# Performance work log

Hardware: AMD Instinct MI355X
Metric: run time of the kernel (lower is better)

Reference implementation:

```python
import jax, jax.numpy as jnp
import numpy as np

BATCH = 4096
NUM_FEATURES = 2048
DEPTH = 4
KERNEL = 2
THRESHOLD = 0.0


def setup_inputs() -> dict:
    key = jax.random.key(0)
    keys = jax.random.split(key, 2 + 2 * DEPTH + 2)
    inp = {}
    inp['x'] = jax.random.normal(keys[0], (BATCH, NUM_FEATURES), dtype=jnp.float32)
    # Conv2d(1,1,kernel_size=2) weight (k,k) and scalar bias, PyTorch-style init scale
    fan_in = KERNEL * KERNEL
    bound = 1.0 / np.sqrt(fan_in)
    inp['conv_w'] = jax.random.uniform(keys[1], (KERNEL, KERNEL), jnp.float32, -bound, bound)
    inp['conv_b'] = jax.random.uniform(keys[2], (), jnp.float32, -bound, bound)
    # MLP hidden layers
    lb = 1.0 / np.sqrt(NUM_FEATURES)
    for i in range(DEPTH):
        inp[f'W{i}'] = jax.random.uniform(keys[3 + 2 * i], (NUM_FEATURES, NUM_FEATURES), jnp.float32, -lb, lb)
        inp[f'b{i}'] = jax.random.uniform(keys[4 + 2 * i], (NUM_FEATURES,), jnp.float32, -lb, lb)
    inp['Wh'] = jax.random.uniform(keys[3 + 2 * DEPTH], (2, NUM_FEATURES), jnp.float32, -lb, lb)
    inp['bh'] = jax.random.uniform(keys[4 + 2 * DEPTH], (2,), jnp.float32, -lb, lb)
    return inp


def reference(x, conv_w, conv_b, W0, b0, W1, b1, W2, b2, W3, b3, Wh, bh):
    # Per-feature ConvFilter on a constant k x k patch of value x_i collapses to
    # sigmoid(x_i * sum(conv_w) + conv_b - threshold)  -- one fused elementwise op.
    h = jax.nn.sigmoid(x * jnp.sum(conv_w) + conv_b - THRESHOLD)  # (B, F)
    for W, b in ((W0, b0), (W1, b1), (W2, b2), (W3, b3)):
        h = jax.nn.relu(h @ W.T + b)
    return h @ Wh.T + bh  # (B, 2)
```

## Files before the change

kernel.cpp:

```cpp
#include <hip/hip_runtime.h>
#include <math.h>

#define BATCH 4096
#define NF    2048

typedef signed char    i8;
typedef unsigned int   u32;
typedef __attribute__((ext_vector_type(4))) int   intx4;
typedef __attribute__((ext_vector_type(4))) float floatx4;

#define LBW 0.022097086912079612f
#define QMAX 32512.0f
#define AMAX_H 3.0f

__global__ __launch_bounds__(256) void prep_kernel(
    const float* __restrict__ x, const float* __restrict__ cw,
    const float* __restrict__ cb,
    const float* __restrict__ w0, const float* __restrict__ w1,
    const float* __restrict__ w2, const float* __restrict__ w3,
    i8* __restrict__ h1o, i8* __restrict__ h2o,
    i8* __restrict__ q1,  i8* __restrict__ q2)
{
    const int bid = blockIdx.x;
    if (bid < 8192) {
        const float s = cw[0] + cw[1] + cw[2] + cw[3];
        const float c = cb[0];
        const int i = bid * 256 + threadIdx.x;
        float4 v = ((const float4*)x)[i];
        float vv[4] = {v.x, v.y, v.z, v.w};
        char4 c1, c2;
        #pragma unroll
        for (int j = 0; j < 4; ++j) {
            float r = 1.0f / (1.0f + expf(-(vv[j] * s + c)));
            int X = (int)(r * QMAX + 0.5f);
            int h1 = (X + 128) >> 8;
            int h2 = X - (h1 << 8);
            ((i8*)&c1)[j] = (i8)h1;
            ((i8*)&c2)[j] = (i8)h2;
        }
        *(char4*)&h1o[(size_t)i * 4] = c1;
        *(char4*)&h2o[(size_t)i * 4] = c2;
    } else {
        const int b2    = bid - 8192;
        const int layer = b2 >> 12;
        const int i     = (b2 & 4095) * 256 + threadIdx.x;
        const float* w = (layer == 0) ? w0 : (layer == 1) ? w1
                       : (layer == 2) ? w2 : w3;
        const size_t base = (size_t)layer * (size_t)NF * NF;
        float4 v = ((const float4*)w)[i];
        float vv[4] = {v.x, v.y, v.z, v.w};
        char4 c1, c2;
        #pragma unroll
        for (int j = 0; j < 4; ++j) {
            int X = (int)floorf(vv[j] * (QMAX / LBW) + 0.5f);
            X = max(-32512, min(32512, X));
            int h1 = (X + 128) >> 8;
            int h2 = X - (h1 << 8);
            ((i8*)&c1)[j] = (i8)h1;
            ((i8*)&c2)[j] = (i8)h2;
        }
        *(char4*)&q1[base + (size_t)i * 4] = c1;
        *(char4*)&q2[base + (size_t)i * 4] = c2;
    }
}

#define BM 256
#define BN 128
#define BK 64

__device__ __forceinline__ void stage16(const void* g, void* l) {
    __builtin_amdgcn_global_load_lds(
        (const __attribute__((address_space(1))) u32*)g,
        (__attribute__((address_space(3))) u32*)l, 16, 0, 0);
}

__global__ __launch_bounds__(512, 2) void gemm_i8_split(
    const i8* __restrict__ A1, const i8* __restrict__ A2,
    const i8* __restrict__ B1, const i8* __restrict__ B2,
    const float* __restrict__ bias,
    i8* __restrict__ C1, i8* __restrict__ C2,
    const float* __restrict__ Wh, const float* __restrict__ bh,
    float* __restrict__ outp,
    float combo, float outscale, int last, int M, int N, int K)
{
    extern __shared__ i8 smem[];
    i8* const sA1 = smem;
    i8* const sA2 = smem + 32768;
    i8* const sB1 = smem + 65536;
    i8* const sB2 = smem + 81920;

    const int t    = threadIdx.x;
    const int wv   = t >> 6;
    const int ln   = t & 63;
    const int quad = ln >> 4;
    const int ml   = ln & 15;
    const int wm   = wv >> 1;
    const int wn   = wv & 1;
    const int bm   = blockIdx.y * BM;
    const int bn   = blockIdx.x * BN;
    const int lnoff = ln * 16;

    int rA0 = (bm + (wv * 2 + 0) * 16 + ml) * K + quad * 16;
    int rA1 = (bm + (wv * 2 + 1) * 16 + ml) * K + quad * 16;
    int rB  = (bn +  wv * 16          + ml) * K + quad * 16;

    intx4 zero = {0, 0, 0, 0};
    intx4 acc11[4][4], accX[4][4];
    #pragma unroll
    for (int i = 0; i < 4; ++i)
        #pragma unroll
        for (int j = 0; j < 4; ++j) { acc11[i][j] = zero; accX[i][j] = zero; }

    stage16(A1 + rA0, sA1 + (wv * 2 + 0) * 1024);
    stage16(A1 + rA1, sA1 + (wv * 2 + 1) * 1024);
    stage16(A2 + rA0, sA2 + (wv * 2 + 0) * 1024);
    stage16(A2 + rA1, sA2 + (wv * 2 + 1) * 1024);
    stage16(B1 + rB,  sB1 + wv * 1024);
    stage16(B2 + rB,  sB2 + wv * 1024);
    rA0 += BK; rA1 += BK; rB += BK;
    asm volatile("s_waitcnt vmcnt(0)" ::: "memory");
    __builtin_amdgcn_s_barrier();
    asm volatile("" ::: "memory");

    intx4 a1f0, a1f1, a2f0, a2f1;
    intx4 b1lo0, b1lo1, b2lo0, b2lo1, b1hi0, b1hi1, b2hi0, b2hi1;

#define LDA_(P, CUR, c) (*(const intx4*)&(P)[(CUR) * 16384 + (c) * 1024 + lnoff])
#define LDB_(P, CUR, c) (*(const intx4*)&(P)[(CUR) * 8192  + (c) * 1024 + lnoff])
#define MFMA3(i, j, A1R, A2R, B1R, B2R) \
    acc11[i][j] = __builtin_amdgcn_mfma_i32_16x16x64_i8(A1R, B1R, acc11[i][j], 0, 0, 0); \
    accX [i][j] = __builtin_amdgcn_mfma_i32_16x16x64_i8(A1R, B2R, accX [i][j], 0, 0, 0); \
    accX [i][j] = __builtin_amdgcn_mfma_i32_16x16x64_i8(A2R, B1R, accX [i][j], 0, 0, 0);
#define FENCE_   asm volatile("" ::: "memory")
#define BARRIER_ FENCE_; __builtin_amdgcn_s_barrier(); FENCE_
#define LGKM0_   asm volatile("s_waitcnt lgkmcnt(0)" ::: "memory")

#define KTILE(CUR, SG) { \
     \
    a1f0 = LDA_(sA1, CUR, wm * 4 + 0);  a1f1 = LDA_(sA1, CUR, wm * 4 + 1); \
    a2f0 = LDA_(sA2, CUR, wm * 4 + 0);  a2f1 = LDA_(sA2, CUR, wm * 4 + 1); \
    b1lo0 = LDB_(sB1, CUR, wn * 4 + 0); b1lo1 = LDB_(sB1, CUR, wn * 4 + 1); \
    b2lo0 = LDB_(sB2, CUR, wn * 4 + 0); b2lo1 = LDB_(sB2, CUR, wn * 4 + 1); \
    if (SG) { stage16(A1 + rA0, sA1 + (1 - (CUR)) * 16384 + (wv * 2 + 0) * 1024); \
              stage16(A1 + rA1, sA1 + (1 - (CUR)) * 16384 + (wv * 2 + 1) * 1024); } \
    BARRIER_; LGKM0_; \
    __builtin_amdgcn_s_setprio(1); \
    MFMA3(0, 0, a1f0, a2f0, b1lo0, b2lo0) MFMA3(0, 1, a1f0, a2f0, b1lo1, b2lo1) \
    MFMA3(1, 0, a1f1, a2f1, b1lo0, b2lo0) MFMA3(1, 1, a1f1, a2f1, b1lo1, b2lo1) \
    __builtin_amdgcn_s_setprio(0); \
    BARRIER_; \
     \
    b1hi0 = LDB_(sB1, CUR, wn * 4 + 2); b1hi1 = LDB_(sB1, CUR, wn * 4 + 3); \
    b2hi0 = LDB_(sB2, CUR, wn * 4 + 2); b2hi1 = LDB_(sB2, CUR, wn * 4 + 3); \
    if (SG) { stage16(A2 + rA0, sA2 + (1 - (CUR)) * 16384 + (wv * 2 + 0) * 1024); \
              stage16(A2 + rA1, sA2 + (1 - (CUR)) * 16384 + (wv * 2 + 1) * 1024); } \
    BARRIER_; LGKM0_; \
    __builtin_amdgcn_s_setprio(1); \
    MFMA3(0, 2, a1f0, a2f0, b1hi0, b2hi0) MFMA3(0, 3, a1f0, a2f0, b1hi1, b2hi1) \
    MFMA3(1, 2, a1f1, a2f1, b1hi0, b2hi0) MFMA3(1, 3, a1f1, a2f1, b1hi1, b2hi1) \
    __builtin_amdgcn_s_setprio(0); \
    BARRIER_; \
     \
    a1f0 = LDA_(sA1, CUR, wm * 4 + 2);  a1f1 = LDA_(sA1, CUR, wm * 4 + 3); \
    a2f0 = LDA_(sA2, CUR, wm * 4 + 2);  a2f1 = LDA_(sA2, CUR, wm * 4 + 3); \
    if (SG) { stage16(B1 + rB, sB1 + (1 - (CUR)) * 8192 + wv * 1024); \
              stage16(B2 + rB, sB2 + (1 - (CUR)) * 8192 + wv * 1024); } \
    rA0 += BK; rA1 += BK; rB += BK; \
    BARRIER_; LGKM0_; \
    __builtin_amdgcn_s_setprio(1); \
    MFMA3(2, 2, a1f0, a2f0, b1hi0, b2hi0) MFMA3(2, 3, a1f0, a2f0, b1hi1, b2hi1) \
    MFMA3(3, 2, a1f1, a2f1, b1hi0, b2hi0) MFMA3(3, 3, a1f1, a2f1, b1hi1, b2hi1) \
    __builtin_amdgcn_s_setprio(0); \
     \
    asm volatile("s_waitcnt vmcnt(0)" ::: "memory"); \
    BARRIER_; \
    __builtin_amdgcn_s_setprio(1); \
    MFMA3(2, 0, a1f0, a2f0, b1lo0, b2lo0) MFMA3(2, 1, a1f0, a2f0, b1lo1, b2lo1) \
    MFMA3(3, 0, a1f1, a2f1, b1lo0, b2lo0) MFMA3(3, 1, a1f1, a2f1, b1lo1, b2lo1) \
    __builtin_amdgcn_s_setprio(0); \
}

    const int NIT = K >> 7;
    #pragma unroll 1
    for (int it = 0; it < NIT; ++it) {
        KTILE(0, 1)
        KTILE(1, (it < NIT - 1))
    }

#undef KTILE
#undef LDA_
#undef LDB_
#undef MFMA3
#undef FENCE_
#undef BARRIER_
#undef LGKM0_

    if (!last) {
        #pragma unroll
        for (int j = 0; j < 4; ++j) {
            const int n  = bn + wn * 64 + j * 16 + ml;
            const float bv = bias[n];
            #pragma unroll
            for (int i = 0; i < 4; ++i) {
                #pragma unroll
                for (int r = 0; r < 4; ++r) {
                    const int m = bm + wm * 64 + i * 16 + quad * 4 + r;
                    float v = fmaf(65536.0f, (float)acc11[i][j][r],
                                   256.0f * (float)accX[i][j][r]) * combo + bv;
                    v = fmaxf(v, 0.0f);
                    int X = (int)(fminf(v * outscale, QMAX) + 0.5f);
                    int h1 = (X + 128) >> 8;
                    int h2 = X - (h1 << 8);
                    C1[(size_t)m * N + n] = (i8)h1;
                    C2[(size_t)m * N + n] = (i8)h2;
                }
            }
        }
    } else {
        float wh0[4], wh1[4], bv[4];
        #pragma unroll
        for (int j = 0; j < 4; ++j) {
            const int n = bn + wn * 64 + j * 16 + ml;
            bv[j]  = bias[n];
            wh0[j] = Wh[n];
            wh1[j] = Wh[NF + n];
        }
        #pragma unroll
        for (int i = 0; i < 4; ++i) {
            #pragma unroll
            for (int r = 0; r < 4; ++r) {
                float s0 = 0.0f, s1 = 0.0f;
                #pragma unroll
                for (int j = 0; j < 4; ++j) {
                    float v = fmaf(65536.0f, (float)acc11[i][j][r],
                                   256.0f * (float)accX[i][j][r]) * combo + bv[j];
                    v = fmaxf(v, 0.0f);
                    s0 = fmaf(v, wh0[j], s0);
                    s1 = fmaf(v, wh1[j], s1);
                }
                #pragma unroll
                for (int off = 8; off > 0; off >>= 1) {
                    s0 += __shfl_xor(s0, off, 64);
                    s1 += __shfl_xor(s1, off, 64);
                }
                if (ml == 0) {
                    const int m = bm + wm * 64 + i * 16 + quad * 4 + r;
                    if (bn == 0 && wn == 0) { s0 += bh[0]; s1 += bh[1]; }
                    atomicAdd(&outp[(size_t)m * 2 + 0], s0);
                    atomicAdd(&outp[(size_t)m * 2 + 1], s1);
                }
            }
        }
    }
}

__global__ __launch_bounds__(256) void act_kernel_f32(
    const float* __restrict__ x, const float* __restrict__ conv_w,
    const float* __restrict__ conv_b, float* __restrict__ h, int n4)
{
    const float s = conv_w[0] + conv_w[1] + conv_w[2] + conv_w[3];
    const float c = conv_b[0];
    int i = blockIdx.x * blockDim.x + threadIdx.x;
    if (i < n4) {
        float4 v = ((const float4*)x)[i];
        float4 r;
        r.x = 1.0f / (1.0f + expf(-(v.x * s + c)));
        r.y = 1.0f / (1.0f + expf(-(v.y * s + c)));
        r.z = 1.0f / (1.0f + expf(-(v.z * s + c)));
        r.w = 1.0f / (1.0f + expf(-(v.w * s + c)));
        ((float4*)h)[i] = r;
    }
}

#define FBM 128
#define FBN 128
#define FBK 16
#define FPAD 4

__global__ __launch_bounds__(256) void gemm_bias_relu_f32(
    const float* __restrict__ A, const float* __restrict__ W,
    const float* __restrict__ bias, float* __restrict__ C,
    int M, int N, int K, int do_relu)
{
    __shared__ float As[FBK][FBM + FPAD];
    __shared__ float Bs[FBK][FBN + FPAD];
    const int t  = threadIdx.x;
    const int bm = blockIdx.y * FBM;
    const int bn = blockIdx.x * FBN;
    const int tn = (t & 15) * 8;
    const int tm = (t >> 4) * 8;
    const int r0 = t >> 2;
    const int kv = (t & 3) << 2;
    float acc[8][8] = {};
    for (int k0 = 0; k0 < K; k0 += FBK) {
        #pragma unroll
        for (int half = 0; half < 2; ++half) {
            const int row = r0 + half * 64;
            float4 av = *(const float4*)&A[(size_t)(bm + row) * K + k0 + kv];
            As[kv + 0][row] = av.x; As[kv + 1][row] = av.y;
            As[kv + 2][row] = av.z; As[kv + 3][row] = av.w;
            float4 bv = *(const float4*)&W[(size_t)(bn + row) * K + k0 + kv];
            Bs[kv + 0][row] = bv.x; Bs[kv + 1][row] = bv.y;
            Bs[kv + 2][row] = bv.z; Bs[kv + 3][row] = bv.w;
        }
        __syncthreads();
        #pragma unroll
        for (int kk = 0; kk < FBK; ++kk) {
            float a[8], b[8];
            *(float4*)&a[0] = *(const float4*)&As[kk][tm];
            *(float4*)&a[4] = *(const float4*)&As[kk][tm + 4];
            *(float4*)&b[0] = *(const float4*)&Bs[kk][tn];
            *(float4*)&b[4] = *(const float4*)&Bs[kk][tn + 4];
            #pragma unroll
            for (int i = 0; i < 8; ++i)
                #pragma unroll
                for (int j = 0; j < 8; ++j)
                    acc[i][j] = fmaf(a[i], b[j], acc[i][j]);
        }
        __syncthreads();
    }
    #pragma unroll
    for (int i = 0; i < 8; ++i) {
        const int row = bm + tm + i;
        #pragma unroll
        for (int j = 0; j < 8; j += 4) {
            float4 v;
            v.x = acc[i][j + 0] + bias[bn + tn + j + 0];
            v.y = acc[i][j + 1] + bias[bn + tn + j + 1];
            v.z = acc[i][j + 2] + bias[bn + tn + j + 2];
            v.w = acc[i][j + 3] + bias[bn + tn + j + 3];
            if (do_relu) {
                v.x = fmaxf(v.x, 0.0f); v.y = fmaxf(v.y, 0.0f);
                v.z = fmaxf(v.z, 0.0f); v.w = fmaxf(v.w, 0.0f);
            }
            *(float4*)&C[(size_t)row * N + bn + tn + j] = v;
        }
    }
}

__global__ __launch_bounds__(256) void head_kernel_f32(
    const float* __restrict__ h, const float* __restrict__ Wh,
    const float* __restrict__ bh, float* __restrict__ out)
{
    const int wave = threadIdx.x >> 6;
    const int lane = threadIdx.x & 63;
    const int row  = blockIdx.x * 4 + wave;
    const float* hr = h + (size_t)row * NF;
    float acc0 = 0.0f, acc1 = 0.0f;
    for (int k = lane * 4; k < NF; k += 256) {
        float4 v  = *(const float4*)&hr[k];
        float4 w0 = *(const float4*)&Wh[k];
        float4 w1 = *(const float4*)&Wh[NF + k];
        acc0 += v.x * w0.x + v.y * w0.y + v.z * w0.z + v.w * w0.w;
        acc1 += v.x * w1.x + v.y * w1.y + v.z * w1.z + v.w * w1.w;
    }
    #pragma unroll
    for (int off = 32; off > 0; off >>= 1) {
        acc0 += __shfl_down(acc0, off, 64);
        acc1 += __shfl_down(acc1, off, 64);
    }
    if (lane == 0) {
        out[row * 2 + 0] = acc0 + bh[0];
        out[row * 2 + 1] = acc1 + bh[1];
    }
}

extern "C" void kernel_launch(void* const* d_in, const int* in_sizes, int n_in,
                              void* d_out, int out_size, void* d_ws, size_t ws_size,
                              hipStream_t stream)
{
    const float* x      = (const float*)d_in[0];
    const float* conv_w = (const float*)d_in[1];
    const float* conv_b = (const float*)d_in[2];
    const float* Ws[4]  = {(const float*)d_in[3], (const float*)d_in[5],
                           (const float*)d_in[7], (const float*)d_in[9]};
    const float* bs[4]  = {(const float*)d_in[4], (const float*)d_in[6],
                           (const float*)d_in[8], (const float*)d_in[10]};
    const float* Wh     = (const float*)d_in[11];
    const float* bh     = (const float*)d_in[12];
    float* out = (float*)d_out;

    const size_t AE = (size_t)BATCH * NF;
    const size_t WE = (size_t)NF * NF;
    const size_t need_i8 = 4 * AE + 8 * WE;

    const int n4 = (BATCH * NF) / 4;

    if (ws_size >= need_i8) {
        static int attr_done = 0;
        if (!attr_done) {
            (void)hipFuncSetAttribute(
                reinterpret_cast<const void*>(gemm_i8_split),
                hipFuncAttributeMaxDynamicSharedMemorySize, 96 * 1024);
            attr_done = 1;
        }

        i8* base = (i8*)d_ws;
        i8* a01 = base;
        i8* a02 = a01 + AE;
        i8* a11 = a02 + AE;
        i8* a12 = a11 + AE;
        i8* wq1 = a12 + AE;
        i8* wq2 = wq1 + 4 * WE;

        hipMemsetAsync(out, 0, (size_t)out_size * sizeof(float), stream);

        prep_kernel<<<8192 + 16384, 256, 0, stream>>>(
            x, conv_w, conv_b, Ws[0], Ws[1], Ws[2], Ws[3],
            a01, a02, wq1, wq2);

        const float sW = LBW / QMAX;
        const float outscale = QMAX / AMAX_H;
        dim3 grid(NF / BN, BATCH / BM);

        i8 *in1 = a01, *in2 = a02, *o1 = a11, *o2 = a12;
        for (int l = 0; l < 4; ++l) {
            const float sA = ((l == 0) ? 1.0f : AMAX_H) / QMAX;
            gemm_i8_split<<<grid, 512, 96 * 1024, stream>>>(
                in1, in2, wq1 + (size_t)l * WE, wq2 + (size_t)l * WE,
                bs[l], o1, o2, Wh, bh, out,
                sA * sW, outscale, (l == 3) ? 1 : 0, BATCH, NF, NF);
            i8* t1 = in1; i8* t2 = in2;
            in1 = o1; in2 = o2; o1 = t1; o2 = t2;
        }
    } else {
        float* ws0 = (float*)d_ws;
        float* ws1 = ws0 + AE;
        act_kernel_f32<<<(n4 + 255) / 256, 256, 0, stream>>>(x, conv_w, conv_b, ws0, n4);
        dim3 fgrid(NF / FBN, BATCH / FBM);
        gemm_bias_relu_f32<<<fgrid, 256, 0, stream>>>(ws0, Ws[0], bs[0], ws1, BATCH, NF, NF, 1);
        gemm_bias_relu_f32<<<fgrid, 256, 0, stream>>>(ws1, Ws[1], bs[1], ws0, BATCH, NF, NF, 1);
        gemm_bias_relu_f32<<<fgrid, 256, 0, stream>>>(ws0, Ws[2], bs[2], ws1, BATCH, NF, NF, 1);
        gemm_bias_relu_f32<<<fgrid, 256, 0, stream>>>(ws1, Ws[3], bs[3], ws0, BATCH, NF, NF, 1);
        head_kernel_f32<<<BATCH / 4, 256, 0, stream>>>(ws0, Wh, bh, out);
    }
}
```

Before: 404.3 us.

## Triple-buffer LDS staging in int8 split GEMM with deeper prefetch

Replaces the double-buffered shared-memory pipeline with a three-stage ring buffer (3 x 48KB), prefetching two K-tiles ahead and waiting with vmcnt(6) so one tile's global loads can remain in flight across iterations. It also restructures the loop to one K-tile per iteration with rotating read/write bases. The aim is to hide global load latency behind MFMA work. LDS use rises from 96KB to 144KB per block, which likely drops occupancy from two blocks per CU to one under __launch_bounds__(512,2).

```diff
diff --git a/kernel.cpp b/kernel.cpp
--- a/kernel.cpp
+++ b/kernel.cpp
@@ -68,6 +68,12 @@
 #define BN 128
 #define BK 64
 
+#define BUFSZ  49152
+#define SEC_A1 0
+#define SEC_A2 16384
+#define SEC_B1 32768
+#define SEC_B2 40960
+
 __device__ __forceinline__ void stage16(const void* g, void* l) {
     __builtin_amdgcn_global_load_lds(
         (const __attribute__((address_space(1))) u32*)g,
@@ -84,10 +90,6 @@
     float combo, float outscale, int last, int M, int N, int K)
 {
     extern __shared__ i8 smem[];
-    i8* const sA1 = smem;
-    i8* const sA2 = smem + 32768;
-    i8* const sB1 = smem + 65536;
-    i8* const sB2 = smem + 81920;
 
     const int t    = threadIdx.x;
     const int wv   = t >> 6;
@@ -111,22 +113,31 @@
         #pragma unroll
         for (int j = 0; j < 4; ++j) { acc11[i][j] = zero; accX[i][j] = zero; }
 
-    stage16(A1 + rA0, sA1 + (wv * 2 + 0) * 1024);
-    stage16(A1 + rA1, sA1 + (wv * 2 + 1) * 1024);
-    stage16(A2 + rA0, sA2 + (wv * 2 + 0) * 1024);
-    stage16(A2 + rA1, sA2 + (wv * 2 + 1) * 1024);
-    stage16(B1 + rB,  sB1 + wv * 1024);
-    stage16(B2 + rB,  sB2 + wv * 1024);
+    stage16(A1 + rA0, smem + 0 * BUFSZ + SEC_A1 + (wv * 2 + 0) * 1024);
+    stage16(A1 + rA1, smem + 0 * BUFSZ + SEC_A1 + (wv * 2 + 1) * 1024);
+    stage16(A2 + rA0, smem + 0 * BUFSZ + SEC_A2 + (wv * 2 + 0) * 1024);
+    stage16(A2 + rA1, smem + 0 * BUFSZ + SEC_A2 + (wv * 2 + 1) * 1024);
+    stage16(B1 + rB,  smem + 0 * BUFSZ + SEC_B1 + wv * 1024);
+    stage16(B2 + rB,  smem + 0 * BUFSZ + SEC_B2 + wv * 1024);
     rA0 += BK; rA1 += BK; rB += BK;
-    asm volatile("s_waitcnt vmcnt(0)" ::: "memory");
+    stage16(A1 + rA0, smem + 1 * BUFSZ + SEC_A1 + (wv * 2 + 0) * 1024);
+    stage16(A1 + rA1, smem + 1 * BUFSZ + SEC_A1 + (wv * 2 + 1) * 1024);
+    stage16(A2 + rA0, smem + 1 * BUFSZ + SEC_A2 + (wv * 2 + 0) * 1024);
+    stage16(A2 + rA1, smem + 1 * BUFSZ + SEC_A2 + (wv * 2 + 1) * 1024);
+    stage16(B1 + rB,  smem + 1 * BUFSZ + SEC_B1 + wv * 1024);
+    stage16(B2 + rB,  smem + 1 * BUFSZ + SEC_B2 + wv * 1024);
+    rA0 += BK; rA1 += BK; rB += BK;
+    asm volatile("s_waitcnt vmcnt(6)" ::: "memory");
     __builtin_amdgcn_s_barrier();
     asm volatile("" ::: "memory");
 
+    int rdbase = 0;
+    int wrbase = 2 * BUFSZ;
+
     intx4 a1f0, a1f1, a2f0, a2f1;
     intx4 b1lo0, b1lo1, b2lo0, b2lo1, b1hi0, b1hi1, b2hi0, b2hi1;
 
-#define LDA_(P, CUR, c) (*(const intx4*)&(P)[(CUR) * 16384 + (c) * 1024 + lnoff])
-#define LDB_(P, CUR, c) (*(const intx4*)&(P)[(CUR) * 8192  + (c) * 1024 + lnoff])
+#define LDA_(SEC, c) (*(const intx4*)&smem[rdbase + (SEC) + (c) * 1024 + lnoff])
 #define MFMA3(i, j, A1R, A2R, B1R, B2R) \
     acc11[i][j] = __builtin_amdgcn_mfma_i32_16x16x64_i8(A1R, B1R, acc11[i][j], 0, 0, 0); \
     accX [i][j] = __builtin_amdgcn_mfma_i32_16x16x64_i8(A1R, B2R, accX [i][j], 0, 0, 0); \
@@ -135,61 +146,58 @@
 #define BARRIER_ FENCE_; __builtin_amdgcn_s_barrier(); FENCE_
 #define LGKM0_   asm volatile("s_waitcnt lgkmcnt(0)" ::: "memory")
 
-#define KTILE(CUR, SG) { \
-     \
-    a1f0 = LDA_(sA1, CUR, wm * 4 + 0);  a1f1 = LDA_(sA1, CUR, wm * 4 + 1); \
-    a2f0 = LDA_(sA2, CUR, wm * 4 + 0);  a2f1 = LDA_(sA2, CUR, wm * 4 + 1); \
-    b1lo0 = LDB_(sB1, CUR, wn * 4 + 0); b1lo1 = LDB_(sB1, CUR, wn * 4 + 1); \
-    b2lo0 = LDB_(sB2, CUR, wn * 4 + 0); b2lo1 = LDB_(sB2, CUR, wn * 4 + 1); \
-    if (SG) { stage16(A1 + rA0, sA1 + (1 - (CUR)) * 16384 + (wv * 2 + 0) * 1024); \
-              stage16(A1 + rA1, sA1 + (1 - (CUR)) * 16384 + (wv * 2 + 1) * 1024); } \
-    BARRIER_; LGKM0_; \
-    __builtin_amdgcn_s_setprio(1); \
-    MFMA3(0, 0, a1f0, a2f0, b1lo0, b2lo0) MFMA3(0, 1, a1f0, a2f0, b1lo1, b2lo1) \
-    MFMA3(1, 0, a1f1, a2f1, b1lo0, b2lo0) MFMA3(1, 1, a1f1, a2f1, b1lo1, b2lo1) \
-    __builtin_amdgcn_s_setprio(0); \
-    BARRIER_; \
-     \
-    b1hi0 = LDB_(sB1, CUR, wn * 4 + 2); b1hi1 = LDB_(sB1, CUR, wn * 4 + 3); \
-    b2hi0 = LDB_(sB2, CUR, wn * 4 + 2); b2hi1 = LDB_(sB2, CUR, wn * 4 + 3); \
-    if (SG) { stage16(A2 + rA0, sA2 + (1 - (CUR)) * 16384 + (wv * 2 + 0) * 1024); \
-              stage16(A2 + rA1, sA2 + (1 - (CUR)) * 16384 + (wv * 2 + 1) * 1024); } \
-    BARRIER_; LGKM0_; \
-    __builtin_amdgcn_s_setprio(1); \
-    MFMA3(0, 2, a1f0, a2f0, b1hi0, b2hi0) MFMA3(0, 3, a1f0, a2f0, b1hi1, b2hi1) \
-    MFMA3(1, 2, a1f1, a2f1, b1hi0, b2hi0) MFMA3(1, 3, a1f1, a2f1, b1hi1, b2hi1) \
-    __builtin_amdgcn_s_setprio(0); \
-    BARRIER_; \
-     \
-    a1f0 = LDA_(sA1, CUR, wm * 4 + 2);  a1f1 = LDA_(sA1, CUR, wm * 4 + 3); \
-    a2f0 = LDA_(sA2, CUR, wm * 4 + 2);  a2f1 = LDA_(sA2, CUR, wm * 4 + 3); \
-    if (SG) { stage16(B1 + rB, sB1 + (1 - (CUR)) * 8192 + wv * 1024); \
-              stage16(B2 + rB, sB2 + (1 - (CUR)) * 8192 + wv * 1024); } \
-    rA0 += BK; rA1 += BK; rB += BK; \
-    BARRIER_; LGKM0_; \
-    __builtin_amdgcn_s_setprio(1); \
-    MFMA3(2, 2, a1f0, a2f0, b1hi0, b2hi0) MFMA3(2, 3, a1f0, a2f0, b1hi1, b2hi1) \
-    MFMA3(3, 2, a1f1, a2f1, b1hi0, b2hi0) MFMA3(3, 3, a1f1, a2f1, b1hi1, b2hi1) \
-    __builtin_amdgcn_s_setprio(0); \
-     \
-    asm volatile("s_waitcnt vmcnt(0)" ::: "memory"); \
-    BARRIER_; \
-    __builtin_amdgcn_s_setprio(1); \
-    MFMA3(2, 0, a1f0, a2f0, b1lo0, b2lo0) MFMA3(2, 1, a1f0, a2f0, b1lo1, b2lo1) \
-    MFMA3(3, 0, a1f1, a2f1, b1lo0, b2lo0) MFMA3(3, 1, a1f1, a2f1, b1lo1, b2lo1) \
-    __builtin_amdgcn_s_setprio(0); \
-}
-
-    const int NIT = K >> 7;
+    const int NIT = K >> 6;
     #pragma unroll 1
-    for (int it = 0; it < NIT; ++it) {
-        KTILE(0, 1)
-        KTILE(1, (it < NIT - 1))
-    }
-
-#undef KTILE
+    for (int kt = 0; kt < NIT; ++kt) {
+        const int sg = (kt < NIT - 2);
+        a1f0 = LDA_(SEC_A1, wm * 4 + 0);  a1f1 = LDA_(SEC_A1, wm * 4 + 1);
+        a2f0 = LDA_(SEC_A2, wm * 4 + 0);  a2f1 = LDA_(SEC_A2, wm * 4 + 1);
+        b1lo0 = LDA_(SEC_B1, wn * 4 + 0); b1lo1 = LDA_(SEC_B1, wn * 4 + 1);
+        b2lo0 = LDA_(SEC_B2, wn * 4 + 0); b2lo1 = LDA_(SEC_B2, wn * 4 + 1);
+        if (sg) {
+            stage16(A1 + rA0, smem + wrbase + SEC_A1 + (wv * 2 + 0) * 1024);
+            stage16(A1 + rA1, smem + wrbase + SEC_A1 + (wv * 2 + 1) * 1024);
+            stage16(A2 + rA0, smem + wrbase + SEC_A2 + (wv * 2 + 0) * 1024);
+            stage16(A2 + rA1, smem + wrbase + SEC_A2 + (wv * 2 + 1) * 1024);
+        }
+        BARRIER_; LGKM0_;
+        __builtin_amdgcn_s_setprio(1);
+        MFMA3(0, 0, a1f0, a2f0, b1lo0, b2lo0) MFMA3(0, 1, a1f0, a2f0, b1lo1, b2lo1)
+        MFMA3(1, 0, a1f1, a2f1, b1lo0, b2lo0) MFMA3(1, 1, a1f1, a2f1, b1lo1, b2lo1)
+        __builtin_amdgcn_s_setprio(0);
+        BARRIER_;
+        b1hi0 = LDA_(SEC_B1, wn * 4 + 2); b1hi1 = LDA_(SEC_B1, wn * 4 + 3);
+        b2hi0 = LDA_(SEC_B2, wn * 4 + 2); b2hi1 = LDA_(SEC_B2, wn * 4 + 3);
+        if (sg) {
+            stage16(B1 + rB, smem + wrbase + SEC_B1 + wv * 1024);
+            stage16(B2 + rB, smem + wrbase + SEC_B2 + wv * 1024);
+            rA0 += BK; rA1 += BK; rB += BK;
+        }
+        BARRIER_; LGKM0_;
+        __builtin_amdgcn_s_setprio(1);
+        MFMA3(0, 2, a1f0, a2f0, b1hi0, b2hi0) MFMA3(0, 3, a1f0, a2f0, b1hi1, b2hi1)
+        MFMA3(1, 2, a1f1, a2f1, b1hi0, b2hi0) MFMA3(1, 3, a1f1, a2f1, b1hi1, b2hi1)
+        __builtin_amdgcn_s_setprio(0);
+        BARRIER_;
+        a1f0 = LDA_(SEC_A1, wm * 4 + 2);  a1f1 = LDA_(SEC_A1, wm * 4 + 3);
+        a2f0 = LDA_(SEC_A2, wm * 4 + 2);  a2f1 = LDA_(SEC_A2, wm * 4 + 3);
+        BARRIER_; LGKM0_;
+        __builtin_amdgcn_s_setprio(1);
+        MFMA3(2, 2, a1f0, a2f0, b1hi0, b2hi0) MFMA3(2, 3, a1f0, a2f0, b1hi1, b2hi1)
+        MFMA3(3, 2, a1f1, a2f1, b1hi0, b2hi0) MFMA3(3, 3, a1f1, a2f1, b1hi1, b2hi1)
+        __builtin_amdgcn_s_setprio(0);
+        if (sg) { asm volatile("s_waitcnt vmcnt(6)" ::: "memory"); }
+        else    { asm volatile("s_waitcnt vmcnt(0)" ::: "memory"); }
+        BARRIER_;
+        __builtin_amdgcn_s_setprio(1);
+        MFMA3(2, 0, a1f0, a2f0, b1lo0, b2lo0) MFMA3(2, 1, a1f0, a2f0, b1lo1, b2lo1)
+        MFMA3(3, 0, a1f1, a2f1, b1lo0, b2lo0) MFMA3(3, 1, a1f1, a2f1, b1lo1, b2lo1)
+        __builtin_amdgcn_s_setprio(0);
+        rdbase = (rdbase == 2 * BUFSZ) ? 0 : rdbase + BUFSZ;
+        wrbase = (wrbase == 2 * BUFSZ) ? 0 : wrbase + BUFSZ;
+    }
+
 #undef LDA_
-#undef LDB_
 #undef MFMA3
 #undef FENCE_
 #undef BARRIER_
@@ -391,7 +399,7 @@
         if (!attr_done) {
             (void)hipFuncSetAttribute(
                 reinterpret_cast<const void*>(gemm_i8_split),
-                hipFuncAttributeMaxDynamicSharedMemorySize, 96 * 1024);
+                hipFuncAttributeMaxDynamicSharedMemorySize, 3 * BUFSZ);
             attr_done = 1;
         }
 
@@ -416,7 +424,7 @@
         i8 *in1 = a01, *in2 = a02, *o1 = a11, *o2 = a12;
         for (int l = 0; l < 4; ++l) {
             const float sA = ((l == 0) ? 1.0f : AMAX_H) / QMAX;
-            gemm_i8_split<<<grid, 512, 96 * 1024, stream>>>(
+            gemm_i8_split<<<grid, 512, 3 * BUFSZ, stream>>>(
                 in1, in2, wq1 + (size_t)l * WE, wq2 + (size_t)l * WE,
                 bs[l], o1, o2, Wh, bh, out,
                 sA * sW, outscale, (l == 3) ? 1 : 0, BATCH, NF, NF);
```

New measurement: 364.1 us. -9.9%, faster.
